# Kernel tuning notes

Measured on AMD Instinct MI355X. Metric: run time of the kernel, lower is better.

Reference implementation:

```python
import jax, jax.numpy as jnp
import numpy as np

LOSS_WEIGHT = 1.0

# Zero-padded shifts implementing PyTorch cross-correlation stencils.
# _shift_w(x, +1)[..., j] = x[..., j+1] (zero outside), etc.

def _shift_w(x, s):
    if s == 1:
        return jnp.pad(x[..., 1:], ((0, 0), (0, 0), (0, 1)))
    return jnp.pad(x[..., :-1], ((0, 0), (0, 0), (1, 0)))


def _shift_h(x, s):
    if s == 1:
        return jnp.pad(x[..., 1:, :], ((0, 0), (0, 1), (0, 0)))
    return jnp.pad(x[..., :-1, :], ((0, 0), (1, 0), (0, 0)))


def _curvature_loss(prob):
    # prob: [B, H, W]. Fused stencil chain equivalent to the 7 tiny conv2d calls.
    lap = (_shift_h(prob, 1) + _shift_h(prob, -1)
           + _shift_w(prob, 1) + _shift_w(prob, -1) - 4.0 * prob)
    gx = _shift_w(lap, 1) - _shift_w(lap, -1)          # dx = [-1, 0, 1]
    gy = _shift_h(lap, 1) - _shift_h(lap, -1)          # dy = [-1, 0, 1]^T
    hxx = 2.0 * gx - _shift_w(gx, 1) - _shift_w(gx, -1)  # dxx = [-1, 2, -1]
    hyy = 2.0 * gy - _shift_h(gy, 1) - _shift_h(gy, -1)  # dyy = [-1, 2, -1]^T
    hxy = _shift_w(gx, 1) - _shift_w(gx, -1)
    numerator = hxx * (1.0 + gy) ** 2 - 2.0 * hxy * gx * gy + hyy * (1.0 + gx) ** 2
    denominator = 2.0 * (1.0 + gx ** 2 + gy ** 2) ** 1.5
    curvature = numerator / denominator
    neg_curv = jnp.maximum(-curvature, 0.0)
    s = jnp.sum(neg_curv, axis=(1, 2))                              # [B]
    c = jnp.sum(neg_curv != 0, axis=(1, 2)).astype(prob.dtype)      # [B]
    # per-sample masked mean, skipped when no negative curvature
    per_sample = jnp.where(c > 0, s / jnp.maximum(c, 1.0), 0.0)
    return jnp.sum(per_sample)


def setup_inputs() -> dict:
    key = jax.random.key(0)
    k1, k2 = jax.random.split(key)
    pred = jax.random.normal(k1, (8, 4, 1024, 1024), dtype=jnp.float32)
    target = jax.random.randint(k2, (8, 1024, 1024), 0, 4, dtype=jnp.int64)
    return {"pred": pred, "target": target}


def reference(pred, target):
    # softmax=True path; num_classes == 4 branch of the original forward
    p = jax.nn.softmax(pred, axis=1)
    prob_1 = p[:, 1]
    prob_2 = p[:, 1] + p[:, 2]
    prob_3 = p[:, 3]
    loss = (_curvature_loss(prob_1) + _curvature_loss(prob_2)
            + _curvature_loss(prob_3))
    return loss * LOSS_WEIGHT
```

## Files before the change

kernel.cpp:

```cpp
#include <hip/hip_runtime.h>


namespace {
constexpr int H = 1024, W = 1024, B = 8;
constexpr int VALID = 120;
constexpr int NSTRIPS = 9;
constexpr int RCHUNK = 16;
constexpr int NCHUNKS = H / RCHUNK;
constexpr int WPB = 4;
constexpr int NTHREADS = 64 * WPB;
constexpr size_t HW = (size_t)H * W;
}

using v2f = __attribute__((ext_vector_type(2))) float;

__device__ __forceinline__ v2f mk2(float a, float b) {
    v2f r; r.x = a; r.y = b; return r;
}

__device__ __forceinline__ float dpp_left(float x) {
    return __builtin_bit_cast(float,
        __builtin_amdgcn_update_dpp(0, __builtin_bit_cast(int, x),
                                    0x138 , 0xf, 0xf, false));
}
__device__ __forceinline__ float dpp_right(float x) {
    return __builtin_bit_cast(float,
        __builtin_amdgcn_update_dpp(0, __builtin_bit_cast(int, x),
                                    0x130 , 0xf, 0xf, false));
}

__global__ void zero_ws_kernel(unsigned int* ws) {
    if (threadIdx.x < 48) ws[threadIdx.x] = 0u;
}

template <bool RE>
__device__ __forceinline__ void load_row4(const float* __restrict__ basep, int row,
                                          v2f o[4]) {
    const int rc = RE ? min(max(row, 0), H - 1) : row;
    const float* p = basep + (size_t)rc * W;
    o[0] = *(const v2f*)p;
    o[1] = *(const v2f*)(p + HW);
    o[2] = *(const v2f*)(p + 2 * HW);
    o[3] = *(const v2f*)(p + 3 * HW);
}

template <bool EDGE>
__device__ __forceinline__ void softmax_pair(const v2f x[4], bool ok0, bool ok1,
                                             v2f p[3]) {
    const float e0x = __expf(x[0].x), e1x = __expf(x[1].x);
    const float e2x = __expf(x[2].x), e3x = __expf(x[3].x);
    const float e0y = __expf(x[0].y), e1y = __expf(x[1].y);
    const float e2y = __expf(x[2].y), e3y = __expf(x[3].y);
    const float ix = __builtin_amdgcn_rcpf(e0x + e1x + e2x + e3x);
    const float iy = __builtin_amdgcn_rcpf(e0y + e1y + e2y + e3y);
    if (EDGE) {
        p[0] = mk2(ok0 ? e1x * ix : 0.f,          ok1 ? e1y * iy : 0.f);
        p[1] = mk2(ok0 ? (e1x + e2x) * ix : 0.f,  ok1 ? (e1y + e2y) * iy : 0.f);
        p[2] = mk2(ok0 ? e3x * ix : 0.f,          ok1 ? e3y * iy : 0.f);
    } else {
        p[0] = mk2(e1x * ix,          e1y * iy);
        p[1] = mk2((e1x + e2x) * ix,  (e1y + e2y) * iy);
        p[2] = mk2(e3x * ix,          e3y * iy);
    }
}

template <bool CE, bool RE>
__device__ __forceinline__ void sweep(const float* __restrict__ pred,
                                      int b, int strip, int chunk, int lane,
                                      v2f sacc[3], unsigned int cacc0[3],
                                      unsigned int cacc1[3]) {
    const int r0 = chunk * RCHUNK;
    const int li0 = 2 * lane;
    const int col0 = strip * VALID - 4 + li0;
    const int col1 = col0 + 1;
    const int colC = CE ? min(max(col0, 0), W - 2) : col0;
    const float* basep = pred + (size_t)b * 4 * HW + colC;

    const bool cOK0 = !CE || ((unsigned)col0 < (unsigned)W);
    const bool cOK1 = !CE || ((unsigned)col1 < (unsigned)W);
    const v2f gxpM = mk2((!CE || (col0 + 1 < W)) ? 1.f : 0.f,
                         (!CE || (col1 + 1 < W)) ? 1.f : 0.f);
    const v2f gxmM = mk2((!CE || (col0 >= 1)) ? 1.f : 0.f,
                         (!CE || (col1 >= 1)) ? 1.f : 0.f);

    v2f P[4][3];
    v2f L[5][3];
    v2f Rr[4][4];

    {
        v2f t[4];
        load_row4<RE>(basep, r0 - 3, t);
        const bool ok = !RE || ((unsigned)(r0 - 3) < (unsigned)H);
        softmax_pair<CE || RE>(t, ok && cOK0, ok && cOK1, P[2]);
        load_row4<RE>(basep, r0 - 2, t);
        const bool ok2 = !RE || ((unsigned)(r0 - 2) < (unsigned)H);
        softmax_pair<CE || RE>(t, ok2 && cOK0, ok2 && cOK1, P[3]);
    }
    load_row4<RE>(basep, r0 - 1, Rr[0]);
    load_row4<RE>(basep, r0 + 0, Rr[1]);
    load_row4<RE>(basep, r0 + 1, Rr[2]);
    load_row4<RE>(basep, r0 + 2, Rr[3]);

#pragma unroll
    for (int i = 0; i < RCHUNK + 4; ++i) {
        const int y = r0 - 4 + i;
        const bool pok = !RE || ((unsigned)(y + 3) < (unsigned)H);
        softmax_pair<CE || RE>(Rr[i % 4], pok && cOK0, pok && cOK1, P[i % 4]);
        if (i < RCHUNK) load_row4<RE>(basep, y + 7, Rr[i % 4]);
        const bool lok = !RE || ((unsigned)(y + 2) < (unsigned)H);
#pragma unroll
        for (int f = 0; f < 3; ++f) {
            const v2f top = P[(i + 2) % 4][f];
            const v2f mid = P[(i + 3) % 4][f];
            const v2f bot = P[i % 4][f];
            const float lft = dpp_left(mid.y);
            const float rgt = dpp_right(mid.x);
            const v2f horiz = mk2(lft, mid.x) + mk2(mid.y, rgt);
            const v2f l = top + bot + horiz - 4.f * mid;
            if (CE || RE) {
                L[i % 5][f] = mk2((lok && cOK0) ? l.x : 0.f,
                                  (lok && cOK1) ? l.y : 0.f);
            } else {
                L[i % 5][f] = l;
            }
        }
        if (i >= 4) {
            const float gypM = (!RE || (y + 1 < H)) ? 1.f : 0.f;
            const float gymM = (!RE || (y >= 1)) ? 1.f : 0.f;
#pragma unroll
            for (int f = 0; f < 3; ++f) {
                const v2f lm2 = L[(i + 1) % 5][f];
                const v2f lm1 = L[(i + 2) % 5][f];
                const v2f lc  = L[(i + 3) % 5][f];
                const v2f lp1 = L[(i + 4) % 5][f];
                const v2f lp2 = L[i % 5][f];
                const float A  = dpp_left(lc.y);
                const float Bm = dpp_left(lc.x);
                const float Bp = dpp_right(lc.x);
                const float Cc = dpp_right(lc.y);
                const v2f c   = lc;
                const v2f gx  = mk2(lc.y, Bp) - mk2(A, lc.x);
                const v2f gy  = lp1 - lm1;
                const v2f gxp = (mk2(Bp, Cc) - c) * gxpM;
                const v2f gxm = (c - mk2(Bm, A)) * gxmM;
                const v2f gyp = (lp2 - c) * gypM;
                const v2f gym = (c - lm2) * gymM;
                const v2f hxx = 2.f * gx - gxp - gxm;
                const v2f hxy = gxp - gxm;
                const v2f hyy = 2.f * gy - gyp - gym;
                const v2f ox = 1.f + gx, oy = 1.f + gy;
                const v2f numer = hxx * oy * oy - 2.f * hxy * (gx * gy)
                                + hyy * ox * ox;
                const v2f xx = 1.f + gx * gx + gy * gy;
                const float rs0 = __builtin_amdgcn_rsqf(xx.x);
                const float rs1 = __builtin_amdgcn_rsqf(xx.y);
                const v2f invden2 = mk2(rs0 * rs0 * rs0, rs1 * rs1 * rs1);
                const v2f curv2 = numer * invden2;
                const v2f negc = mk2(fmaxf(-curv2.x, 0.f),
                                     fmaxf(-curv2.y, 0.f));
                sacc[f] += negc;
                cacc0[f] += (negc.x != 0.f) ? 1u : 0u;
                cacc1[f] += (negc.y != 0.f) ? 1u : 0u;
            }
        }
    }
}

__global__ __launch_bounds__(NTHREADS, 4)
void curvature_sweep(const float* __restrict__ pred,
                     float* __restrict__ s_ws,
                     unsigned int* __restrict__ c_ws) {
    __shared__ float redS[3][WPB];
    __shared__ unsigned int redC[3][WPB];

    const int strip = blockIdx.x;
    const int b = blockIdx.z;
    const int tid = threadIdx.x;
    const int wv = tid >> 6, lane = tid & 63;
    const int chunk = blockIdx.y * WPB + wv;

    const bool ce = (strip == 0) || (strip == NSTRIPS - 1);
    const bool re = (chunk == 0) || (chunk == NCHUNKS - 1);

    v2f sacc[3] = {mk2(0.f, 0.f), mk2(0.f, 0.f), mk2(0.f, 0.f)};
    unsigned int cacc0[3] = {0u, 0u, 0u};
    unsigned int cacc1[3] = {0u, 0u, 0u};
    if (!ce && !re)
        sweep<false, false>(pred, b, strip, chunk, lane, sacc, cacc0, cacc1);
    else if (ce && !re)
        sweep<true, false>(pred, b, strip, chunk, lane, sacc, cacc0, cacc1);
    else if (!ce && re)
        sweep<false, true>(pred, b, strip, chunk, lane, sacc, cacc0, cacc1);
    else
        sweep<true, true>(pred, b, strip, chunk, lane, sacc, cacc0, cacc1);

    const int col0 = strip * VALID - 4 + 2 * lane;
    const bool gOK = (lane >= 2) && (lane <= 61) && (col0 < W);

#pragma unroll
    for (int f = 0; f < 3; ++f) {
        float v = gOK ? 0.5f * (sacc[f].x + sacc[f].y) : 0.f;
        unsigned int c = gOK ? (cacc0[f] + cacc1[f]) : 0u;
        for (int off = 32; off > 0; off >>= 1) {
            v += __shfl_xor(v, off, 64);
            c += __shfl_xor(c, off, 64);
        }
        if (lane == 0) { redS[f][wv] = v; redC[f][wv] = c; }
    }
    __syncthreads();
    if (tid < 3) {
        float v = 0.f;
        unsigned int c = 0;
        for (int w2 = 0; w2 < WPB; ++w2) { v += redS[tid][w2]; c += redC[tid][w2]; }
        atomicAdd(&s_ws[b * 3 + tid], v);
        atomicAdd(&c_ws[b * 3 + tid], c);
    }
}

__global__ void finalize_kernel(const float* __restrict__ s_ws,
                                const unsigned int* __restrict__ c_ws,
                                float* __restrict__ out) {
    const int lane = threadIdx.x;
    float v = 0.f;
    if (lane < 24) {
        const float s = s_ws[lane];
        const unsigned int c = c_ws[lane];
        v = (c > 0) ? s / (float)c : 0.f;
    }
    for (int off = 32; off > 0; off >>= 1) v += __shfl_down(v, off, 64);
    if (lane == 0) out[0] = v;
}

extern "C" void kernel_launch(void* const* d_in, const int* in_sizes, int n_in,
                              void* d_out, int out_size, void* d_ws, size_t ws_size,
                              hipStream_t stream) {
    const float* pred = (const float*)d_in[0];
    float* s_ws = (float*)d_ws;
    unsigned int* c_ws = (unsigned int*)((char*)d_ws + 24 * sizeof(float));
    float* out = (float*)d_out;

    hipLaunchKernelGGL(zero_ws_kernel, dim3(1), dim3(64), 0, stream,
                       (unsigned int*)d_ws);
    dim3 grid(NSTRIPS, NCHUNKS / WPB, B);
    hipLaunchKernelGGL(curvature_sweep, grid, dim3(NTHREADS), 0, stream,
                       pred, s_ws, c_ws);
    hipLaunchKernelGGL(finalize_kernel, dim3(1), dim3(64), 0, stream,
                       s_ws, c_ws, out);
}
```

Baseline: 56.55 us.

## Scalarize stencil math, shrink prefetch ring, drop atomics and zero kernel

Replaces packed v2f math with scalar floats. The softmax is rewritten relative to x0 so it needs three exps per column instead of four, and the curvature uses one rsq of xx^3 instead of rsq followed by a cube. The row prefetch ring shrinks from 4 rows to 2 and the P ring from 4 to 3, and launch bounds drop to 3 waves per EU. Per-block partial sums are written to distinct slots and reduced by a 256-thread finalize kernel, which removes the zeroing kernel and the global atomics. The shallower prefetch may expose more load latency. The exp(x-x0) form can overflow for large logit differences.

```diff
diff --git a/kernel.cpp b/kernel.cpp
--- a/kernel.cpp
+++ b/kernel.cpp
@@ -9,65 +9,74 @@
 constexpr int NCHUNKS = H / RCHUNK;
 constexpr int WPB = 4;
 constexpr int NTHREADS = 64 * WPB;
+constexpr int NYG = NCHUNKS / WPB;
+constexpr int NBLOCKS = NSTRIPS * NYG * B;
+constexpr int SPG = NSTRIPS * NYG;
 constexpr size_t HW = (size_t)H * W;
-}
-
-using v2f = __attribute__((ext_vector_type(2))) float;
-
-__device__ __forceinline__ v2f mk2(float a, float b) {
-    v2f r; r.x = a; r.y = b; return r;
 }
 
 __device__ __forceinline__ float dpp_left(float x) {
     return __builtin_bit_cast(float,
         __builtin_amdgcn_update_dpp(0, __builtin_bit_cast(int, x),
-                                    0x138 , 0xf, 0xf, false));
+                                    0x138 , 0xf, 0xf, true));
 }
 __device__ __forceinline__ float dpp_right(float x) {
     return __builtin_bit_cast(float,
         __builtin_amdgcn_update_dpp(0, __builtin_bit_cast(int, x),
-                                    0x130 , 0xf, 0xf, false));
-}
-
-__global__ void zero_ws_kernel(unsigned int* ws) {
-    if (threadIdx.x < 48) ws[threadIdx.x] = 0u;
+                                    0x130 , 0xf, 0xf, true));
 }
 
 template <bool RE>
 __device__ __forceinline__ void load_row4(const float* __restrict__ basep, int row,
-                                          v2f o[4]) {
+                                          float2 o[4]) {
     const int rc = RE ? min(max(row, 0), H - 1) : row;
     const float* p = basep + (size_t)rc * W;
-    o[0] = *(const v2f*)p;
-    o[1] = *(const v2f*)(p + HW);
-    o[2] = *(const v2f*)(p + 2 * HW);
-    o[3] = *(const v2f*)(p + 3 * HW);
+    o[0] = *(const float2*)p;
+    o[1] = *(const float2*)(p + HW);
+    o[2] = *(const float2*)(p + 2 * HW);
+    o[3] = *(const float2*)(p + 3 * HW);
 }
 
 template <bool EDGE>
-__device__ __forceinline__ void softmax_pair(const v2f x[4], bool ok0, bool ok1,
-                                             v2f p[3]) {
-    const float e0x = __expf(x[0].x), e1x = __expf(x[1].x);
-    const float e2x = __expf(x[2].x), e3x = __expf(x[3].x);
-    const float e0y = __expf(x[0].y), e1y = __expf(x[1].y);
-    const float e2y = __expf(x[2].y), e3y = __expf(x[3].y);
-    const float ix = __builtin_amdgcn_rcpf(e0x + e1x + e2x + e3x);
-    const float iy = __builtin_amdgcn_rcpf(e0y + e1y + e2y + e3y);
+__device__ __forceinline__ void softmax_col(float x0, float x1, float x2, float x3,
+                                            bool ok, float& p1, float& p12,
+                                            float& p3) {
+    const float e1 = __expf(x1 - x0);
+    const float e2 = __expf(x2 - x0);
+    const float e3 = __expf(x3 - x0);
+    const float t12 = e1 + e2;
+    const float inv = __builtin_amdgcn_rcpf(1.f + (t12 + e3));
     if (EDGE) {
-        p[0] = mk2(ok0 ? e1x * ix : 0.f,          ok1 ? e1y * iy : 0.f);
-        p[1] = mk2(ok0 ? (e1x + e2x) * ix : 0.f,  ok1 ? (e1y + e2y) * iy : 0.f);
-        p[2] = mk2(ok0 ? e3x * ix : 0.f,          ok1 ? e3y * iy : 0.f);
+        p1  = ok ? e1 * inv : 0.f;
+        p12 = ok ? t12 * inv : 0.f;
+        p3  = ok ? e3 * inv : 0.f;
     } else {
-        p[0] = mk2(e1x * ix,          e1y * iy);
-        p[1] = mk2((e1x + e2x) * ix,  (e1y + e2y) * iy);
-        p[2] = mk2(e3x * ix,          e3y * iy);
-    }
+        p1 = e1 * inv; p12 = t12 * inv; p3 = e3 * inv;
+    }
+}
+
+__device__ __forceinline__ void acc_col(float gx, float gy, float gxp, float gxm,
+                                        float gyp, float gym,
+                                        float& s, unsigned int& c) {
+    const float hxx = 2.f * gx - gxp - gxm;
+    const float hxy = gxp - gxm;
+    const float hyy = 2.f * gy - gyp - gym;
+    const float ox = 1.f + gx, oy = 1.f + gy;
+    const float numer = hxx * oy * oy - 2.f * hxy * gx * gy + hyy * ox * ox;
+    const float xx = 1.f + gx * gx + gy * gy;
+    const float xx3 = xx * xx * xx;
+    const float rs = __builtin_amdgcn_rsqf(xx3);
+    const float c2 = numer * rs;
+    const float ng = fmaxf(-c2, 0.f);
+    s += ng;
+    c += (ng != 0.f) ? 1u : 0u;
 }
 
 template <bool CE, bool RE>
 __device__ __forceinline__ void sweep(const float* __restrict__ pred,
                                       int b, int strip, int chunk, int lane,
-                                      v2f sacc[3], unsigned int cacc0[3],
+                                      float sacc0[3], float sacc1[3],
+                                      unsigned int cacc0[3],
                                       unsigned int cacc1[3]) {
     const int r0 = chunk * RCHUNK;
     const int li0 = 2 * lane;
@@ -78,98 +87,101 @@
 
     const bool cOK0 = !CE || ((unsigned)col0 < (unsigned)W);
     const bool cOK1 = !CE || ((unsigned)col1 < (unsigned)W);
-    const v2f gxpM = mk2((!CE || (col0 + 1 < W)) ? 1.f : 0.f,
-                         (!CE || (col1 + 1 < W)) ? 1.f : 0.f);
-    const v2f gxmM = mk2((!CE || (col0 >= 1)) ? 1.f : 0.f,
-                         (!CE || (col1 >= 1)) ? 1.f : 0.f);
-
-    v2f P[4][3];
-    v2f L[5][3];
-    v2f Rr[4][4];
+    const float gxpM0 = (!CE || (col0 + 1 < W)) ? 1.f : 0.f;
+    const float gxpM1 = (!CE || (col1 + 1 < W)) ? 1.f : 0.f;
+    const float gxmM0 = (!CE || (col0 >= 1)) ? 1.f : 0.f;
+    const float gxmM1 = (!CE || (col1 >= 1)) ? 1.f : 0.f;
+
+    float P[3][3][2];
+    float L[5][3][2];
+    float2 Rr[2][4];
 
     {
-        v2f t[4];
+        float2 t[4];
         load_row4<RE>(basep, r0 - 3, t);
         const bool ok = !RE || ((unsigned)(r0 - 3) < (unsigned)H);
-        softmax_pair<CE || RE>(t, ok && cOK0, ok && cOK1, P[2]);
+        softmax_col<CE || RE>(t[0].x, t[1].x, t[2].x, t[3].x, ok && cOK0,
+                              P[1][0][0], P[1][1][0], P[1][2][0]);
+        softmax_col<CE || RE>(t[0].y, t[1].y, t[2].y, t[3].y, ok && cOK1,
+                              P[1][0][1], P[1][1][1], P[1][2][1]);
         load_row4<RE>(basep, r0 - 2, t);
         const bool ok2 = !RE || ((unsigned)(r0 - 2) < (unsigned)H);
-        softmax_pair<CE || RE>(t, ok2 && cOK0, ok2 && cOK1, P[3]);
+        softmax_col<CE || RE>(t[0].x, t[1].x, t[2].x, t[3].x, ok2 && cOK0,
+                              P[2][0][0], P[2][1][0], P[2][2][0]);
+        softmax_col<CE || RE>(t[0].y, t[1].y, t[2].y, t[3].y, ok2 && cOK1,
+                              P[2][0][1], P[2][1][1], P[2][2][1]);
     }
     load_row4<RE>(basep, r0 - 1, Rr[0]);
     load_row4<RE>(basep, r0 + 0, Rr[1]);
-    load_row4<RE>(basep, r0 + 1, Rr[2]);
-    load_row4<RE>(basep, r0 + 2, Rr[3]);
 
 #pragma unroll
     for (int i = 0; i < RCHUNK + 4; ++i) {
         const int y = r0 - 4 + i;
         const bool pok = !RE || ((unsigned)(y + 3) < (unsigned)H);
-        softmax_pair<CE || RE>(Rr[i % 4], pok && cOK0, pok && cOK1, P[i % 4]);
-        if (i < RCHUNK) load_row4<RE>(basep, y + 7, Rr[i % 4]);
+        softmax_col<CE || RE>(Rr[i % 2][0].x, Rr[i % 2][1].x, Rr[i % 2][2].x,
+                              Rr[i % 2][3].x, pok && cOK0,
+                              P[i % 3][0][0], P[i % 3][1][0], P[i % 3][2][0]);
+        softmax_col<CE || RE>(Rr[i % 2][0].y, Rr[i % 2][1].y, Rr[i % 2][2].y,
+                              Rr[i % 2][3].y, pok && cOK1,
+                              P[i % 3][0][1], P[i % 3][1][1], P[i % 3][2][1]);
+        if (i < RCHUNK + 2) load_row4<RE>(basep, y + 5, Rr[i % 2]);
         const bool lok = !RE || ((unsigned)(y + 2) < (unsigned)H);
 #pragma unroll
         for (int f = 0; f < 3; ++f) {
-            const v2f top = P[(i + 2) % 4][f];
-            const v2f mid = P[(i + 3) % 4][f];
-            const v2f bot = P[i % 4][f];
-            const float lft = dpp_left(mid.y);
-            const float rgt = dpp_right(mid.x);
-            const v2f horiz = mk2(lft, mid.x) + mk2(mid.y, rgt);
-            const v2f l = top + bot + horiz - 4.f * mid;
+            const float topx = P[(i + 1) % 3][f][0], topy = P[(i + 1) % 3][f][1];
+            const float midx = P[(i + 2) % 3][f][0], midy = P[(i + 2) % 3][f][1];
+            const float botx = P[i % 3][f][0],       boty = P[i % 3][f][1];
+            const float lft = dpp_left(midy);
+            const float rgt = dpp_right(midx);
+            float lx = (topx + botx) + (lft + midy) - 4.f * midx;
+            float ly = (topy + boty) + (midx + rgt) - 4.f * midy;
             if (CE || RE) {
-                L[i % 5][f] = mk2((lok && cOK0) ? l.x : 0.f,
-                                  (lok && cOK1) ? l.y : 0.f);
-            } else {
-                L[i % 5][f] = l;
+                lx = (lok && cOK0) ? lx : 0.f;
+                ly = (lok && cOK1) ? ly : 0.f;
             }
+            L[i % 5][f][0] = lx;
+            L[i % 5][f][1] = ly;
         }
         if (i >= 4) {
             const float gypM = (!RE || (y + 1 < H)) ? 1.f : 0.f;
             const float gymM = (!RE || (y >= 1)) ? 1.f : 0.f;
 #pragma unroll
             for (int f = 0; f < 3; ++f) {
-                const v2f lm2 = L[(i + 1) % 5][f];
-                const v2f lm1 = L[(i + 2) % 5][f];
-                const v2f lc  = L[(i + 3) % 5][f];
-                const v2f lp1 = L[(i + 4) % 5][f];
-                const v2f lp2 = L[i % 5][f];
-                const float A  = dpp_left(lc.y);
-                const float Bm = dpp_left(lc.x);
-                const float Bp = dpp_right(lc.x);
-                const float Cc = dpp_right(lc.y);
-                const v2f c   = lc;
-                const v2f gx  = mk2(lc.y, Bp) - mk2(A, lc.x);
-                const v2f gy  = lp1 - lm1;
-                const v2f gxp = (mk2(Bp, Cc) - c) * gxpM;
-                const v2f gxm = (c - mk2(Bm, A)) * gxmM;
-                const v2f gyp = (lp2 - c) * gypM;
-                const v2f gym = (c - lm2) * gymM;
-                const v2f hxx = 2.f * gx - gxp - gxm;
-                const v2f hxy = gxp - gxm;
-                const v2f hyy = 2.f * gy - gyp - gym;
-                const v2f ox = 1.f + gx, oy = 1.f + gy;
-                const v2f numer = hxx * oy * oy - 2.f * hxy * (gx * gy)
-                                + hyy * ox * ox;
-                const v2f xx = 1.f + gx * gx + gy * gy;
-                const float rs0 = __builtin_amdgcn_rsqf(xx.x);
-                const float rs1 = __builtin_amdgcn_rsqf(xx.y);
-                const v2f invden2 = mk2(rs0 * rs0 * rs0, rs1 * rs1 * rs1);
-                const v2f curv2 = numer * invden2;
-                const v2f negc = mk2(fmaxf(-curv2.x, 0.f),
-                                     fmaxf(-curv2.y, 0.f));
-                sacc[f] += negc;
-                cacc0[f] += (negc.x != 0.f) ? 1u : 0u;
-                cacc1[f] += (negc.y != 0.f) ? 1u : 0u;
+                const float lcx = L[(i + 3) % 5][f][0];
+                const float lcy = L[(i + 3) % 5][f][1];
+                const float A  = dpp_left(lcy);
+                const float Bm = dpp_left(lcx);
+                const float Bp = dpp_right(lcx);
+                const float Cc = dpp_right(lcy);
+                const float gxx = lcy - A;
+                const float gxy = Bp - lcx;
+                float gxpx = gxy,       gxpy = Cc - lcy;
+                float gxmx = lcx - Bm,  gxmy = gxx;
+                if (CE) {
+                    gxpx *= gxpM0; gxpy *= gxpM1;
+                    gxmx *= gxmM0; gxmy *= gxmM1;
+                }
+                const float gyx = L[(i + 4) % 5][f][0] - L[(i + 2) % 5][f][0];
+                const float gyy = L[(i + 4) % 5][f][1] - L[(i + 2) % 5][f][1];
+                float gypx = L[i % 5][f][0] - lcx;
+                float gypy = L[i % 5][f][1] - lcy;
+                float gymx = lcx - L[(i + 1) % 5][f][0];
+                float gymy = lcy - L[(i + 1) % 5][f][1];
+                if (RE) {
+                    gypx *= gypM; gypy *= gypM;
+                    gymx *= gymM; gymy *= gymM;
+                }
+                acc_col(gxx, gyx, gxpx, gxmx, gypx, gymx, sacc0[f], cacc0[f]);
+                acc_col(gxy, gyy, gxpy, gxmy, gypy, gymy, sacc1[f], cacc1[f]);
             }
         }
     }
 }
 
-__global__ __launch_bounds__(NTHREADS, 4)
+__global__ __launch_bounds__(NTHREADS, 3)
 void curvature_sweep(const float* __restrict__ pred,
-                     float* __restrict__ s_ws,
-                     unsigned int* __restrict__ c_ws) {
+                     float* __restrict__ S_ws,
+                     unsigned int* __restrict__ C_ws) {
     __shared__ float redS[3][WPB];
     __shared__ unsigned int redC[3][WPB];
 
@@ -182,24 +194,23 @@
     const bool ce = (strip == 0) || (strip == NSTRIPS - 1);
     const bool re = (chunk == 0) || (chunk == NCHUNKS - 1);
 
-    v2f sacc[3] = {mk2(0.f, 0.f), mk2(0.f, 0.f), mk2(0.f, 0.f)};
-    unsigned int cacc0[3] = {0u, 0u, 0u};
-    unsigned int cacc1[3] = {0u, 0u, 0u};
+    float sacc0[3] = {0.f, 0.f, 0.f}, sacc1[3] = {0.f, 0.f, 0.f};
+    unsigned int cacc0[3] = {0u, 0u, 0u}, cacc1[3] = {0u, 0u, 0u};
     if (!ce && !re)
-        sweep<false, false>(pred, b, strip, chunk, lane, sacc, cacc0, cacc1);
+        sweep<false, false>(pred, b, strip, chunk, lane, sacc0, sacc1, cacc0, cacc1);
     else if (ce && !re)
-        sweep<true, false>(pred, b, strip, chunk, lane, sacc, cacc0, cacc1);
+        sweep<true, false>(pred, b, strip, chunk, lane, sacc0, sacc1, cacc0, cacc1);
     else if (!ce && re)
-        sweep<false, true>(pred, b, strip, chunk, lane, sacc, cacc0, cacc1);
+        sweep<false, true>(pred, b, strip, chunk, lane, sacc0, sacc1, cacc0, cacc1);
     else
-        sweep<true, true>(pred, b, strip, chunk, lane, sacc, cacc0, cacc1);
+        sweep<true, true>(pred, b, strip, chunk, lane, sacc0, sacc1, cacc0, cacc1);
 
     const int col0 = strip * VALID - 4 + 2 * lane;
     const bool gOK = (lane >= 2) && (lane <= 61) && (col0 < W);
 
 #pragma unroll
     for (int f = 0; f < 3; ++f) {
-        float v = gOK ? 0.5f * (sacc[f].x + sacc[f].y) : 0.f;
+        float v = gOK ? 0.5f * (sacc0[f] + sacc1[f]) : 0.f;
         unsigned int c = gOK ? (cacc0[f] + cacc1[f]) : 0u;
         for (int off = 32; off > 0; off >>= 1) {
             v += __shfl_xor(v, off, 64);
@@ -212,38 +223,61 @@
         float v = 0.f;
         unsigned int c = 0;
         for (int w2 = 0; w2 < WPB; ++w2) { v += redS[tid][w2]; c += redC[tid][w2]; }
-        atomicAdd(&s_ws[b * 3 + tid], v);
-        atomicAdd(&c_ws[b * 3 + tid], c);
-    }
-}
-
-__global__ void finalize_kernel(const float* __restrict__ s_ws,
-                                const unsigned int* __restrict__ c_ws,
-                                float* __restrict__ out) {
-    const int lane = threadIdx.x;
-    float v = 0.f;
-    if (lane < 24) {
-        const float s = s_ws[lane];
-        const unsigned int c = c_ws[lane];
-        v = (c > 0) ? s / (float)c : 0.f;
-    }
-    for (int off = 32; off > 0; off >>= 1) v += __shfl_down(v, off, 64);
-    if (lane == 0) out[0] = v;
+        const int bid = (b * NYG + blockIdx.y) * NSTRIPS + strip;
+        S_ws[bid * 3 + tid] = v;
+        C_ws[bid * 3 + tid] = c;
+    }
+}
+
+__global__ __launch_bounds__(256)
+void finalize_kernel(const float* __restrict__ S_ws,
+                     const unsigned int* __restrict__ C_ws,
+                     float* __restrict__ out) {
+    __shared__ float ls[8][32];
+    __shared__ unsigned int lcn[8][32];
+    __shared__ float qv[32];
+    const int t = threadIdx.x;
+    const int g = t & 31;
+    const int j = t >> 5;
+    float s = 0.f;
+    unsigned int c = 0;
+    if (g < 24) {
+        const int b = g / 3, f = g - 3 * b;
+        const int base = b * SPG;
+        for (int m = 0; m < SPG / 8; ++m) {
+            const int k = base + j * (SPG / 8) + m;
+            s += S_ws[k * 3 + f];
+            c += C_ws[k * 3 + f];
+        }
+    }
+    ls[j][g] = s;
+    lcn[j][g] = c;
+    __syncthreads();
+    if (t < 32) {
+        float ss = 0.f;
+        unsigned int cc = 0;
+        for (int r = 0; r < 8; ++r) { ss += ls[r][t]; cc += lcn[r][t]; }
+        qv[t] = (cc > 0) ? ss / (float)cc : 0.f;
+    }
+    __syncthreads();
+    if (t == 0) {
+        float tot = 0.f;
+        for (int g2 = 0; g2 < 24; ++g2) tot += qv[g2];
+        out[0] = tot;
+    }
 }
 
 extern "C" void kernel_launch(void* const* d_in, const int* in_sizes, int n_in,
                               void* d_out, int out_size, void* d_ws, size_t ws_size,
                               hipStream_t stream) {
     const float* pred = (const float*)d_in[0];
-    float* s_ws = (float*)d_ws;
-    unsigned int* c_ws = (unsigned int*)((char*)d_ws + 24 * sizeof(float));
+    float* S_ws = (float*)d_ws;
+    unsigned int* C_ws = (unsigned int*)((char*)d_ws + NBLOCKS * 3 * sizeof(float));
     float* out = (float*)d_out;
 
-    hipLaunchKernelGGL(zero_ws_kernel, dim3(1), dim3(64), 0, stream,
-                       (unsigned int*)d_ws);
-    dim3 grid(NSTRIPS, NCHUNKS / WPB, B);
+    dim3 grid(NSTRIPS, NYG, B);
     hipLaunchKernelGGL(curvature_sweep, grid, dim3(NTHREADS), 0, stream,
-                       pred, s_ws, c_ws);
-    hipLaunchKernelGGL(finalize_kernel, dim3(1), dim3(64), 0, stream,
-                       s_ws, c_ws, out);
-}
+                       pred, S_ws, C_ws);
+    hipLaunchKernelGGL(finalize_kernel, dim3(1), dim3(256), 0, stream,
+                       S_ws, C_ws, out);
+}
```

Result: slower. 93.20 us (+64.8%).

## Drop zero kernel and atomics, halve block size, cheaper softmax and rsqrt

Applied to the files above, without the earlier changes.

Each block now writes its partial sums and counts to its own workspace slot. A wider finalize kernel reduces all of them, which removes the zeroing kernel launch and the global atomics. Blocks shrink from 4 to 2 waves, doubling the grid. The softmax is rewritten relative to channel 0, dropping one exp per pixel pair, and the curvature denominator takes a single rsqrt of the cubed value instead of cubing the rsqrt. DPP bound_ctrl is also flipped. The rsqrt of a cube can overflow for large gradients, and the finalize kernel now reads thousands of partials.

```diff
diff --git a/kernel.cpp b/kernel.cpp
--- a/kernel.cpp
+++ b/kernel.cpp
@@ -7,8 +7,11 @@
 constexpr int NSTRIPS = 9;
 constexpr int RCHUNK = 16;
 constexpr int NCHUNKS = H / RCHUNK;
-constexpr int WPB = 4;
+constexpr int WPB = 2;
 constexpr int NTHREADS = 64 * WPB;
+constexpr int NYG = NCHUNKS / WPB;
+constexpr int NBLOCKS = NSTRIPS * NYG * B;
+constexpr int SPG = NSTRIPS * NYG;
 constexpr size_t HW = (size_t)H * W;
 }
 
@@ -21,16 +24,12 @@
 __device__ __forceinline__ float dpp_left(float x) {
     return __builtin_bit_cast(float,
         __builtin_amdgcn_update_dpp(0, __builtin_bit_cast(int, x),
-                                    0x138 , 0xf, 0xf, false));
+                                    0x138 , 0xf, 0xf, true));
 }
 __device__ __forceinline__ float dpp_right(float x) {
     return __builtin_bit_cast(float,
         __builtin_amdgcn_update_dpp(0, __builtin_bit_cast(int, x),
-                                    0x130 , 0xf, 0xf, false));
-}
-
-__global__ void zero_ws_kernel(unsigned int* ws) {
-    if (threadIdx.x < 48) ws[threadIdx.x] = 0u;
+                                    0x130 , 0xf, 0xf, true));
 }
 
 template <bool RE>
@@ -47,20 +46,20 @@
 template <bool EDGE>
 __device__ __forceinline__ void softmax_pair(const v2f x[4], bool ok0, bool ok1,
                                              v2f p[3]) {
-    const float e0x = __expf(x[0].x), e1x = __expf(x[1].x);
-    const float e2x = __expf(x[2].x), e3x = __expf(x[3].x);
-    const float e0y = __expf(x[0].y), e1y = __expf(x[1].y);
-    const float e2y = __expf(x[2].y), e3y = __expf(x[3].y);
-    const float ix = __builtin_amdgcn_rcpf(e0x + e1x + e2x + e3x);
-    const float iy = __builtin_amdgcn_rcpf(e0y + e1y + e2y + e3y);
+    const float e1x = __expf(x[1].x - x[0].x), e1y = __expf(x[1].y - x[0].y);
+    const float e2x = __expf(x[2].x - x[0].x), e2y = __expf(x[2].y - x[0].y);
+    const float e3x = __expf(x[3].x - x[0].x), e3y = __expf(x[3].y - x[0].y);
+    const float t12x = e1x + e2x, t12y = e1y + e2y;
+    const float ix = __builtin_amdgcn_rcpf(1.f + (t12x + e3x));
+    const float iy = __builtin_amdgcn_rcpf(1.f + (t12y + e3y));
     if (EDGE) {
-        p[0] = mk2(ok0 ? e1x * ix : 0.f,          ok1 ? e1y * iy : 0.f);
-        p[1] = mk2(ok0 ? (e1x + e2x) * ix : 0.f,  ok1 ? (e1y + e2y) * iy : 0.f);
-        p[2] = mk2(ok0 ? e3x * ix : 0.f,          ok1 ? e3y * iy : 0.f);
+        p[0] = mk2(ok0 ? e1x * ix : 0.f,   ok1 ? e1y * iy : 0.f);
+        p[1] = mk2(ok0 ? t12x * ix : 0.f,  ok1 ? t12y * iy : 0.f);
+        p[2] = mk2(ok0 ? e3x * ix : 0.f,   ok1 ? e3y * iy : 0.f);
     } else {
-        p[0] = mk2(e1x * ix,          e1y * iy);
-        p[1] = mk2((e1x + e2x) * ix,  (e1y + e2y) * iy);
-        p[2] = mk2(e3x * ix,          e3y * iy);
+        p[0] = mk2(e1x * ix,   e1y * iy);
+        p[1] = mk2(t12x * ix,  t12y * iy);
+        p[2] = mk2(e3x * ix,   e3y * iy);
     }
 }
 
@@ -116,13 +115,11 @@
             const float lft = dpp_left(mid.y);
             const float rgt = dpp_right(mid.x);
             const v2f horiz = mk2(lft, mid.x) + mk2(mid.y, rgt);
-            const v2f l = top + bot + horiz - 4.f * mid;
+            v2f l = top + bot + horiz - 4.f * mid;
             if (CE || RE) {
-                L[i % 5][f] = mk2((lok && cOK0) ? l.x : 0.f,
-                                  (lok && cOK1) ? l.y : 0.f);
-            } else {
-                L[i % 5][f] = l;
+                l = mk2((lok && cOK0) ? l.x : 0.f, (lok && cOK1) ? l.y : 0.f);
             }
+            L[i % 5][f] = l;
         }
         if (i >= 4) {
             const float gypM = (!RE || (y + 1 < H)) ? 1.f : 0.f;
@@ -152,15 +149,17 @@
                 const v2f numer = hxx * oy * oy - 2.f * hxy * (gx * gy)
                                 + hyy * ox * ox;
                 const v2f xx = 1.f + gx * gx + gy * gy;
-                const float rs0 = __builtin_amdgcn_rsqf(xx.x);
-                const float rs1 = __builtin_amdgcn_rsqf(xx.y);
-                const v2f invden2 = mk2(rs0 * rs0 * rs0, rs1 * rs1 * rs1);
-                const v2f curv2 = numer * invden2;
-                const v2f negc = mk2(fmaxf(-curv2.x, 0.f),
-                                     fmaxf(-curv2.y, 0.f));
-                sacc[f] += negc;
-                cacc0[f] += (negc.x != 0.f) ? 1u : 0u;
-                cacc1[f] += (negc.y != 0.f) ? 1u : 0u;
+                const v2f xx3 = xx * xx * xx;
+                const float rs0 = __builtin_amdgcn_rsqf(xx3.x);
+                const float rs1 = __builtin_amdgcn_rsqf(xx3.y);
+                const float c2x = numer.x * rs0;
+                const float c2y = numer.y * rs1;
+                const float ngx = fmaxf(-c2x, 0.f);
+                const float ngy = fmaxf(-c2y, 0.f);
+                sacc[f].x += ngx;
+                sacc[f].y += ngy;
+                cacc0[f] += (ngx != 0.f) ? 1u : 0u;
+                cacc1[f] += (ngy != 0.f) ? 1u : 0u;
             }
         }
     }
@@ -168,8 +167,8 @@
 
 __global__ __launch_bounds__(NTHREADS, 4)
 void curvature_sweep(const float* __restrict__ pred,
-                     float* __restrict__ s_ws,
-                     unsigned int* __restrict__ c_ws) {
+                     float* __restrict__ S_ws,
+                     unsigned int* __restrict__ C_ws) {
     __shared__ float redS[3][WPB];
     __shared__ unsigned int redC[3][WPB];
 
@@ -212,38 +211,61 @@
         float v = 0.f;
         unsigned int c = 0;
         for (int w2 = 0; w2 < WPB; ++w2) { v += redS[tid][w2]; c += redC[tid][w2]; }
-        atomicAdd(&s_ws[b * 3 + tid], v);
-        atomicAdd(&c_ws[b * 3 + tid], c);
-    }
-}
-
-__global__ void finalize_kernel(const float* __restrict__ s_ws,
-                                const unsigned int* __restrict__ c_ws,
-                                float* __restrict__ out) {
-    const int lane = threadIdx.x;
-    float v = 0.f;
-    if (lane < 24) {
-        const float s = s_ws[lane];
-        const unsigned int c = c_ws[lane];
-        v = (c > 0) ? s / (float)c : 0.f;
-    }
-    for (int off = 32; off > 0; off >>= 1) v += __shfl_down(v, off, 64);
-    if (lane == 0) out[0] = v;
+        const int bid = (b * NYG + blockIdx.y) * NSTRIPS + strip;
+        S_ws[bid * 3 + tid] = v;
+        C_ws[bid * 3 + tid] = c;
+    }
+}
+
+__global__ __launch_bounds__(256)
+void finalize_kernel(const float* __restrict__ S_ws,
+                     const unsigned int* __restrict__ C_ws,
+                     float* __restrict__ out) {
+    __shared__ float ls[8][32];
+    __shared__ unsigned int lcn[8][32];
+    __shared__ float qv[32];
+    const int t = threadIdx.x;
+    const int g = t & 31;
+    const int j = t >> 5;
+    float s = 0.f;
+    unsigned int c = 0;
+    if (g < 24) {
+        const int b = g / 3, f = g - 3 * b;
+        const int base = b * SPG;
+        for (int m = 0; m < SPG / 8; ++m) {
+            const int k = base + j * (SPG / 8) + m;
+            s += S_ws[k * 3 + f];
+            c += C_ws[k * 3 + f];
+        }
+    }
+    ls[j][g] = s;
+    lcn[j][g] = c;
+    __syncthreads();
+    if (t < 32) {
+        float ss = 0.f;
+        unsigned int cc = 0;
+        for (int r = 0; r < 8; ++r) { ss += ls[r][t]; cc += lcn[r][t]; }
+        qv[t] = (cc > 0) ? ss / (float)cc : 0.f;
+    }
+    __syncthreads();
+    if (t == 0) {
+        float tot = 0.f;
+        for (int g2 = 0; g2 < 24; ++g2) tot += qv[g2];
+        out[0] = tot;
+    }
 }
 
 extern "C" void kernel_launch(void* const* d_in, const int* in_sizes, int n_in,
                               void* d_out, int out_size, void* d_ws, size_t ws_size,
                               hipStream_t stream) {
     const float* pred = (const float*)d_in[0];
-    float* s_ws = (float*)d_ws;
-    unsigned int* c_ws = (unsigned int*)((char*)d_ws + 24 * sizeof(float));
+    float* S_ws = (float*)d_ws;
+    unsigned int* C_ws = (unsigned int*)((char*)d_ws + NBLOCKS * 3 * sizeof(float));
     float* out = (float*)d_out;
 
-    hipLaunchKernelGGL(zero_ws_kernel, dim3(1), dim3(64), 0, stream,
-                       (unsigned int*)d_ws);
-    dim3 grid(NSTRIPS, NCHUNKS / WPB, B);
+    dim3 grid(NSTRIPS, NYG, B);
     hipLaunchKernelGGL(curvature_sweep, grid, dim3(NTHREADS), 0, stream,
-                       pred, s_ws, c_ws);
-    hipLaunchKernelGGL(finalize_kernel, dim3(1), dim3(64), 0, stream,
-                       s_ws, c_ws, out);
-}
+                       pred, S_ws, C_ws);
+    hipLaunchKernelGGL(finalize_kernel, dim3(1), dim3(256), 0, stream,
+                       S_ws, C_ws, out);
+}
```

After: 56.66 us. About the same (+0.2%).
